# Kernel optimization log

Measured on AMD Instinct MI355X. Metric: run time of the kernel, lower is better.

## Reference

```python
import jax, jax.numpy as jnp
import numpy as np

L = 64        # label_size = len(label2id)
START = 62    # label2id['START']
STOP = 63     # label2id['STOP']
T = 200000    # sequence length
NEG = -10000.0


def setup_inputs() -> dict:
    key = jax.random.key(0)
    k1, k2 = jax.random.split(key)
    lstm_feats = jax.random.normal(k1, (1, T, L), dtype=jnp.float32)
    transitions = jax.random.normal(k2, (L, L), dtype=jnp.float32)
    # CRF constructor masks: cannot transition INTO START, cannot transition FROM STOP
    transitions = transitions.at[START, :].set(NEG).at[:, STOP].set(NEG)
    return {"lstm_feats": lstm_feats, "transitions": transitions}


def reference(lstm_feats, transitions):
    # Viterbi decode, vectorized over tags; lax.scan over time replaces the
    # nested Python loops of the original (same recurrence, same math).
    feats = lstm_feats[0]  # (T, L)
    init = jnp.full((L,), NEG, dtype=lstm_feats.dtype).at[START].set(0.0)

    def step(v, feat):
        # scores[next, prev] = v[prev] + transitions[next, prev]
        scores = v[None, :] + transitions          # (L, L)
        bp = jnp.argmax(scores, axis=1).astype(jnp.int32)  # backpointers per next_tag
        v_new = jnp.max(scores, axis=1) + feat     # viterbi vars + emission
        return v_new, bp

    v, bptrs = jax.lax.scan(step, init, feats)     # bptrs: (T, L)

    terminal = v + transitions[STOP]               # (L,)
    best = jnp.argmax(terminal).astype(jnp.int32)
    path_score = terminal[best]

    # Backtrack: reverse scan emits the tag chosen at each time step, in order.
    def back(tag, bp):
        return bp[tag], tag

    _, best_path = jax.lax.scan(back, best, bptrs, reverse=True)  # (T,) int32
    return path_score, best_path
```

## Files before the change

kernel.cpp:

```cpp
#include <hip/hip_runtime.h>

#define L 64
#define TLEN 200000
#define CH 528
#define NCH 379
#define LASTLEN (TLEN - (NCH - 1) * CH)
#define MAINT 199992
#define NEGV -10000.0f
#define STARTT 62
#define STOPT 63

#define CKPT_OFF 0
#define M_OFF ((NCH + 1) * L * 4)
#define ETAG_OFF (M_OFF + NCH * L)

typedef float f32x4 __attribute__((ext_vector_type(4)));

#define WAVE_BARRIER() __asm__ volatile("s_waitcnt lgkmcnt(0)\ns_barrier" ::: "memory")
#define FAST_BARRIER() __asm__ volatile("s_barrier" ::: "memory")
#define STEP_BARRIER() __asm__ volatile("" ::: "memory")

__device__ __forceinline__ float max3f(float a, float b, float c) {
    float r;
    __asm__("v_max3_f32 %0, %1, %2, %3" : "=v"(r) : "v"(a), "v"(b), "v"(c));
    return r;
}

__global__ __launch_bounds__(256, 1) void k_forward(const float* __restrict__ feats,
                                                    const float* __restrict__ trans,
                                                    float* __restrict__ ckpt) {
    const int tid = threadIdx.x;
    const int n = tid & 63;
    const int w = tid >> 6;

    const f32x4* t4 = reinterpret_cast<const f32x4*>(trans) + n * 16 + w * 4;
    f32x4 q0 = t4[0], q1 = t4[1], q2 = t4[2], q3 = t4[3];
    __asm__ volatile("" : "+v"(q0), "+v"(q1), "+v"(q2), "+v"(q3));

    __shared__ __align__(16) float vbuf[3][L];

    vbuf[0][n] = (n == STARTT) ? 0.0f : NEGV;
    vbuf[1][n] = -INFINITY;
    vbuf[2][n] = -INFINITY;
    WAVE_BARRIER();

    float fc[6];
#pragma unroll
    for (int j = 0; j < 6; ++j) fc[j] = feats[j * L + n];

    int nextck = 0, cidx = 0;

#define FWD_STEP(RD, WR, RS, FEAT)                                            \
    do {                                                                      \
        if (w == 0) vbuf[RS][n] = -INFINITY;                                  \
        const f32x4 va0 = *reinterpret_cast<const f32x4*>(&vbuf[RD][16 * w + 0]);  \
        const f32x4 va1 = *reinterpret_cast<const f32x4*>(&vbuf[RD][16 * w + 4]);  \
        const f32x4 va2 = *reinterpret_cast<const f32x4*>(&vbuf[RD][16 * w + 8]);  \
        const f32x4 va3 = *reinterpret_cast<const f32x4*>(&vbuf[RD][16 * w + 12]); \
        const f32x4 s0 = va0 + q0, s1 = va1 + q1, s2 = va2 + q2, s3 = va3 + q3;    \
        const float m0 = max3f(fmaxf(s0.x, s0.y), s0.z, s0.w);                \
        const float m1 = max3f(fmaxf(s1.x, s1.y), s1.z, s1.w);                \
        const float m2 = max3f(fmaxf(s2.x, s2.y), s2.z, s2.w);                \
        const float m3 = max3f(fmaxf(s3.x, s3.y), s3.z, s3.w);                \
        const float cand = fmaxf(max3f(m0, m1, m2), m3) + (FEAT);             \
        __hip_atomic_fetch_max(&vbuf[WR][n], cand, __ATOMIC_RELAXED,          \
                               __HIP_MEMORY_SCOPE_WORKGROUP);                 \
        FAST_BARRIER();                                                       \
    } while (0)

    for (int tb = 0; tb < MAINT; tb += 6) {
        if (tb == nextck) {
            if (w == 0) ckpt[cidx * L + n] = vbuf[0][n];
            nextck += CH;
            ++cidx;
        }
        float fn_[6];
        const bool more = (tb + 6) < MAINT;
        if (more) {
#pragma unroll
            for (int j = 0; j < 6; ++j) fn_[j] = feats[(tb + 6 + j) * L + n];
        }
        FWD_STEP(0, 1, 2, fc[0]);
        FWD_STEP(1, 2, 0, fc[1]);
        FWD_STEP(2, 0, 1, fc[2]);
        FWD_STEP(0, 1, 2, fc[3]);
        FWD_STEP(1, 2, 0, fc[4]);
        FWD_STEP(2, 0, 1, fc[5]);
        if (more) {
#pragma unroll
            for (int j = 0; j < 6; ++j) fc[j] = fn_[j];
        }
    }

    float ft[8];
#pragma unroll
    for (int j = 0; j < 8; ++j) ft[j] = feats[(MAINT + j) * L + n];
    FWD_STEP(0, 1, 2, ft[0]);
    FWD_STEP(1, 2, 0, ft[1]);
    FWD_STEP(2, 0, 1, ft[2]);
    FWD_STEP(0, 1, 2, ft[3]);
    FWD_STEP(1, 2, 0, ft[4]);
    FWD_STEP(2, 0, 1, ft[5]);
    FWD_STEP(0, 1, 2, ft[6]);
    FWD_STEP(1, 2, 0, ft[7]);
    if (w == 0) ckpt[NCH * L + n] = vbuf[2][n];
#undef FWD_STEP
}

__device__ __forceinline__ void load_trow(const float* __restrict__ trans, int n, float* trow) {
#pragma unroll
    for (int i = 0; i < 16; ++i) {
        const f32x4 q = reinterpret_cast<const f32x4*>(trans)[n * 16 + i];
        trow[4 * i + 0] = q.x;
        trow[4 * i + 1] = q.y;
        trow[4 * i + 2] = q.z;
        trow[4 * i + 3] = q.w;
    }
}

__device__ __forceinline__ void replay_chunk(const float* __restrict__ feats,
                                             const float* __restrict__ ckpt,
                                             const float* trow, float* vsh,
                                             unsigned char* bpl, int c, int len, int n) {
    float vreg = ckpt[c * L + n];
    vsh[n] = vreg;
    STEP_BARRIER();
    const int base = c * CH;

    float fc[8];
#pragma unroll
    for (int j = 0; j < 8; ++j) fc[j] = feats[(base + j) * L + n];

    for (int sb = 0; sb < len; sb += 8) {
        float fn_[8];
        const bool more = (sb + 8) < len;
        if (more) {
#pragma unroll
            for (int j = 0; j < 8; ++j) fn_[j] = feats[(base + sb + 8 + j) * L + n];
        }
#pragma unroll
        for (int j = 0; j < 8; ++j) {
            float mc[4];
            int ic[4];
#pragma unroll
            for (int g = 0; g < 4; ++g) {
                float m = -INFINITY;
                int idx = g * 16;
#pragma unroll
                for (int r = 0; r < 4; ++r) {
                    const int pb = g * 16 + r * 4;
                    const f32x4 vv = *reinterpret_cast<const f32x4*>(vsh + pb);
                    const float a = vv.x + trow[pb + 0];
                    const float b = vv.y + trow[pb + 1];
                    const float cc = vv.z + trow[pb + 2];
                    const float d = vv.w + trow[pb + 3];
                    if (a > m)  { m = a;  idx = pb + 0; }
                    if (b > m)  { m = b;  idx = pb + 1; }
                    if (cc > m) { m = cc; idx = pb + 2; }
                    if (d > m)  { m = d;  idx = pb + 3; }
                }
                mc[g] = m;
                ic[g] = idx;
            }
            float m = mc[0];
            int idx = ic[0];
            if (mc[1] > m) { m = mc[1]; idx = ic[1]; }
            if (mc[2] > m) { m = mc[2]; idx = ic[2]; }
            if (mc[3] > m) { m = mc[3]; idx = ic[3]; }

            vreg = m + fc[j];
            bpl[(sb + j) * L + n] = (unsigned char)idx;
            vsh[n] = vreg;
            STEP_BARRIER();
        }
        if (more) {
#pragma unroll
            for (int j = 0; j < 8; ++j) fc[j] = fn_[j];
        }
    }
}

__global__ __launch_bounds__(64, 1) void k_maps(const float* __restrict__ feats,
                                                const float* __restrict__ trans,
                                                const float* __restrict__ ckpt,
                                                unsigned char* __restrict__ M) {
    const int c = blockIdx.x;
    const int n = threadIdx.x;
    const int len = (c == NCH - 1) ? LASTLEN : CH;

    __shared__ __align__(16) float vsh[L];
    __shared__ unsigned char bpl[CH * L];

    float trow[L];
    load_trow(trans, n, trow);
    replay_chunk(feats, ckpt, trow, vsh, bpl, c, len, n);
    __syncthreads();

    int tag = n;
    for (int s = len - 1; s >= 0; --s) tag = bpl[s * L + tag];
    M[c * L + n] = (unsigned char)tag;
}

__global__ __launch_bounds__(64, 1) void k_stitch(const float* __restrict__ trans,
                                                  const float* __restrict__ ckpt,
                                                  const unsigned char* __restrict__ M,
                                                  int* __restrict__ etag,
                                                  float* __restrict__ out) {
    const int n = threadIdx.x;
    __shared__ float tsh[L];
    __shared__ int bsh;
    __shared__ __align__(16) unsigned char msh[NCH * L];

    tsh[n] = ckpt[NCH * L + n] + trans[STOPT * L + n];
    __syncthreads();
    if (n == 0) {
        float m = tsh[0];
        int b = 0;
        for (int p = 1; p < L; ++p)
            if (tsh[p] > m) { m = tsh[p]; b = p; }
        out[0] = m;
        bsh = b;
    }
    __syncthreads();

    for (int i = n; i < (NCH * L) / 4; i += L)
        reinterpret_cast<int*>(msh)[i] = reinterpret_cast<const int*>(M)[i];
    __syncthreads();

    if (n == 0) {
        int carry = bsh;
        for (int c = NCH - 1; c >= 1; --c) {
            etag[c] = carry;
            carry = msh[c * L + carry];
        }
        etag[0] = carry;
    }
}

__global__ __launch_bounds__(64, 1) void k_emit(const float* __restrict__ feats,
                                                const float* __restrict__ trans,
                                                const float* __restrict__ ckpt,
                                                const int* __restrict__ etag,
                                                float* __restrict__ out) {
    const int c = blockIdx.x;
    const int n = threadIdx.x;
    const int len = (c == NCH - 1) ? LASTLEN : CH;

    __shared__ __align__(16) float vsh[L];
    __shared__ unsigned char bpl[CH * L];
    __shared__ unsigned char plc[CH];

    float trow[L];
    load_trow(trans, n, trow);
    replay_chunk(feats, ckpt, trow, vsh, bpl, c, len, n);
    __syncthreads();

    int tag = etag[c];
    for (int s = len - 1; s >= 0; --s) {
        if (n == 0) plc[s] = (unsigned char)tag;
        tag = bpl[s * L + tag];
    }
    __syncthreads();

    for (int i = n; i < len; i += L)
        out[1 + c * CH + i] = (float)plc[i];
}

extern "C" void kernel_launch(void* const* d_in, const int* in_sizes, int n_in,
                              void* d_out, int out_size, void* d_ws, size_t ws_size,
                              hipStream_t stream) {
    const float* feats = (const float*)d_in[0];
    const float* trans = (const float*)d_in[1];
    float* out = (float*)d_out;
    char* ws = (char*)d_ws;
    float* ckpt = (float*)(ws + CKPT_OFF);
    unsigned char* M = (unsigned char*)(ws + M_OFF);
    int* etag = (int*)(ws + ETAG_OFF);

    hipLaunchKernelGGL(k_forward, dim3(1), dim3(256), 0, stream, feats, trans, ckpt);
    hipLaunchKernelGGL(k_maps, dim3(NCH), dim3(64), 0, stream, feats, trans, ckpt, M);
    hipLaunchKernelGGL(k_stitch, dim3(1), dim3(64), 0, stream, trans, ckpt, M, etag, out);
    hipLaunchKernelGGL(k_emit, dim3(NCH), dim3(64), 0, stream, feats, trans, ckpt, etag, out);
}
```

Baseline: 30.15 ms.

## Replace LDS atomic-max Viterbi step with readlane broadcast and partial-max exchange

The forward recurrence no longer keeps the viterbi vector in shared memory, where it was updated with workgroup-scoped atomic max and reset every step. Each wave now holds its 16 previous-tag values in registers and broadcasts them with readlane. Each lane computes a partial max over those 16 tags, writes it to a double-buffered, swizzled LDS slot, passes one barrier, then reads and combines the four partials plus the emission. This takes the atomic RMW and the buffer reset off the serial per-step critical path, at the cost of 16 readlane operations per step. The unroll also goes from 6 to 8 steps, which removes the separate tail section.

```diff
diff --git a/kernel.cpp b/kernel.cpp
--- a/kernel.cpp
+++ b/kernel.cpp
@@ -5,7 +5,6 @@
 #define CH 528
 #define NCH 379
 #define LASTLEN (TLEN - (NCH - 1) * CH)
-#define MAINT 199992
 #define NEGV -10000.0f
 #define STARTT 62
 #define STOPT 63
@@ -16,7 +15,6 @@
 
 typedef float f32x4 __attribute__((ext_vector_type(4)));
 
-#define WAVE_BARRIER() __asm__ volatile("s_waitcnt lgkmcnt(0)\ns_barrier" ::: "memory")
 #define FAST_BARRIER() __asm__ volatile("s_barrier" ::: "memory")
 #define STEP_BARRIER() __asm__ volatile("" ::: "memory")
 
@@ -26,84 +24,92 @@
     return r;
 }
 
+#define RL(v, k) __int_as_float(__builtin_amdgcn_readlane(__float_as_int(v), k))
+
 __global__ __launch_bounds__(256, 1) void k_forward(const float* __restrict__ feats,
                                                     const float* __restrict__ trans,
                                                     float* __restrict__ ckpt) {
     const int tid = threadIdx.x;
-    const int n = tid & 63;
+    const int l = tid & 63;
     const int w = tid >> 6;
+    const int n = l;
+    const int pcol = 16 * w + (l & 15);
+    const int wswz = (w + (n >> 2)) & 3;
 
     const f32x4* t4 = reinterpret_cast<const f32x4*>(trans) + n * 16 + w * 4;
     f32x4 q0 = t4[0], q1 = t4[1], q2 = t4[2], q3 = t4[3];
     __asm__ volatile("" : "+v"(q0), "+v"(q1), "+v"(q2), "+v"(q3));
 
-    __shared__ __align__(16) float vbuf[3][L];
-
-    vbuf[0][n] = (n == STARTT) ? 0.0f : NEGV;
-    vbuf[1][n] = -INFINITY;
-    vbuf[2][n] = -INFINITY;
-    WAVE_BARRIER();
-
-    float fc[6];
-#pragma unroll
-    for (int j = 0; j < 6; ++j) fc[j] = feats[j * L + n];
+    __shared__ __align__(16) float pm[2][L][4];
+
+    float vcomb = (pcol == STARTT) ? 0.0f : NEGV;
+
+    float fc[8];
+#pragma unroll
+    for (int j = 0; j < 8; ++j) fc[j] = feats[j * L + pcol];
 
     int nextck = 0, cidx = 0;
 
-#define FWD_STEP(RD, WR, RS, FEAT)                                            \
-    do {                                                                      \
-        if (w == 0) vbuf[RS][n] = -INFINITY;                                  \
-        const f32x4 va0 = *reinterpret_cast<const f32x4*>(&vbuf[RD][16 * w + 0]);  \
-        const f32x4 va1 = *reinterpret_cast<const f32x4*>(&vbuf[RD][16 * w + 4]);  \
-        const f32x4 va2 = *reinterpret_cast<const f32x4*>(&vbuf[RD][16 * w + 8]);  \
-        const f32x4 va3 = *reinterpret_cast<const f32x4*>(&vbuf[RD][16 * w + 12]); \
-        const f32x4 s0 = va0 + q0, s1 = va1 + q1, s2 = va2 + q2, s3 = va3 + q3;    \
-        const float m0 = max3f(fmaxf(s0.x, s0.y), s0.z, s0.w);                \
-        const float m1 = max3f(fmaxf(s1.x, s1.y), s1.z, s1.w);                \
-        const float m2 = max3f(fmaxf(s2.x, s2.y), s2.z, s2.w);                \
-        const float m3 = max3f(fmaxf(s3.x, s3.y), s3.z, s3.w);                \
-        const float cand = fmaxf(max3f(m0, m1, m2), m3) + (FEAT);             \
-        __hip_atomic_fetch_max(&vbuf[WR][n], cand, __ATOMIC_RELAXED,          \
-                               __HIP_MEMORY_SCOPE_WORKGROUP);                 \
-        FAST_BARRIER();                                                       \
+#define FWD_STEP(BUF, FEAT)                                                    \
+    do {                                                                       \
+                         \
+        const float s0 = RL(vcomb, 0),  s1 = RL(vcomb, 1);                     \
+        const float s2 = RL(vcomb, 2),  s3 = RL(vcomb, 3);                     \
+        const float s4 = RL(vcomb, 4),  s5 = RL(vcomb, 5);                     \
+        const float s6 = RL(vcomb, 6),  s7 = RL(vcomb, 7);                     \
+        const float s8 = RL(vcomb, 8),  s9 = RL(vcomb, 9);                     \
+        const float s10 = RL(vcomb, 10), s11 = RL(vcomb, 11);                  \
+        const float s12 = RL(vcomb, 12), s13 = RL(vcomb, 13);                  \
+        const float s14 = RL(vcomb, 14), s15 = RL(vcomb, 15);                  \
+                     \
+        const float c0 = s0 + q0.x,  c1 = s1 + q0.y;                           \
+        const float c2 = s2 + q0.z,  c3 = s3 + q0.w;                           \
+        const float c4 = s4 + q1.x,  c5 = s5 + q1.y;                           \
+        const float c6 = s6 + q1.z,  c7 = s7 + q1.w;                           \
+        const float c8 = s8 + q2.x,  c9 = s9 + q2.y;                           \
+        const float c10 = s10 + q2.z, c11 = s11 + q2.w;                        \
+        const float c12 = s12 + q3.x, c13 = s13 + q3.y;                        \
+        const float c14 = s14 + q3.z, c15 = s15 + q3.w;                        \
+        const float a0 = max3f(c0, c1, c2);                                    \
+        const float a1 = max3f(c3, c4, c5);                                    \
+        const float a2 = max3f(c6, c7, c8);                                    \
+        const float a3 = max3f(c9, c10, c11);                                  \
+        const float a4 = max3f(c12, c13, c14);                                 \
+        const float pmv = fmaxf(max3f(a0, a1, a2), max3f(a3, a4, c15));        \
+                                       \
+        pm[BUF][n][wswz] = pmv;                                                \
+        FAST_BARRIER();                                                        \
+                       \
+        const f32x4 pq = *reinterpret_cast<const f32x4*>(&pm[BUF][pcol][0]);   \
+        vcomb = fmaxf(max3f(pq.x, pq.y, pq.z), pq.w) + (FEAT);                 \
     } while (0)
 
-    for (int tb = 0; tb < MAINT; tb += 6) {
+    for (int tb = 0; tb < TLEN; tb += 8) {
         if (tb == nextck) {
-            if (w == 0) ckpt[cidx * L + n] = vbuf[0][n];
+            if (l < 16) ckpt[cidx * L + 16 * w + l] = vcomb;
             nextck += CH;
             ++cidx;
         }
-        float fn_[6];
-        const bool more = (tb + 6) < MAINT;
-        if (more) {
-#pragma unroll
-            for (int j = 0; j < 6; ++j) fn_[j] = feats[(tb + 6 + j) * L + n];
-        }
-        FWD_STEP(0, 1, 2, fc[0]);
-        FWD_STEP(1, 2, 0, fc[1]);
-        FWD_STEP(2, 0, 1, fc[2]);
-        FWD_STEP(0, 1, 2, fc[3]);
-        FWD_STEP(1, 2, 0, fc[4]);
-        FWD_STEP(2, 0, 1, fc[5]);
-        if (more) {
-#pragma unroll
-            for (int j = 0; j < 6; ++j) fc[j] = fn_[j];
-        }
-    }
-
-    float ft[8];
-#pragma unroll
-    for (int j = 0; j < 8; ++j) ft[j] = feats[(MAINT + j) * L + n];
-    FWD_STEP(0, 1, 2, ft[0]);
-    FWD_STEP(1, 2, 0, ft[1]);
-    FWD_STEP(2, 0, 1, ft[2]);
-    FWD_STEP(0, 1, 2, ft[3]);
-    FWD_STEP(1, 2, 0, ft[4]);
-    FWD_STEP(2, 0, 1, ft[5]);
-    FWD_STEP(0, 1, 2, ft[6]);
-    FWD_STEP(1, 2, 0, ft[7]);
-    if (w == 0) ckpt[NCH * L + n] = vbuf[2][n];
+        float fn_[8];
+        const bool more = (tb + 8) < TLEN;
+        if (more) {
+#pragma unroll
+            for (int j = 0; j < 8; ++j) fn_[j] = feats[(tb + 8 + j) * L + pcol];
+        }
+        FWD_STEP(0, fc[0]);
+        FWD_STEP(1, fc[1]);
+        FWD_STEP(0, fc[2]);
+        FWD_STEP(1, fc[3]);
+        FWD_STEP(0, fc[4]);
+        FWD_STEP(1, fc[5]);
+        FWD_STEP(0, fc[6]);
+        FWD_STEP(1, fc[7]);
+        if (more) {
+#pragma unroll
+            for (int j = 0; j < 8; ++j) fc[j] = fn_[j];
+        }
+    }
+    if (l < 16) ckpt[NCH * L + 16 * w + l] = vcomb;
 #undef FWD_STEP
 }
 
```

New measurement: 36.67 ms. +21.6%, slower.
